# Kernel optimization log

Measured on AMD Instinct MI355X. Metric: run time of the kernel, lower is better.

## Reference

```python
import jax, jax.numpy as jnp
import numpy as np

EMBED_DIM = 768
NUM_HEADS = 12
HEAD_DIM = EMBED_DIM // NUM_HEADS
B, T = 2, 2048


def setup_inputs() -> dict:
    key = jax.random.key(0)
    kx, kq, kqb, ko, kob = jax.random.split(key, 5)
    x = jax.random.normal(kx, (B, T, EMBED_DIM), dtype=jnp.float32)
    # xavier-uniform style params
    lim_qkv = float(np.sqrt(6.0 / (EMBED_DIM + 3 * EMBED_DIM)))
    qkv_kernel = jax.random.uniform(kq, (EMBED_DIM, 3 * EMBED_DIM), minval=-lim_qkv, maxval=lim_qkv, dtype=jnp.float32)
    qkv_bias = jnp.zeros((3 * EMBED_DIM,), dtype=jnp.float32)
    lim_o = float(np.sqrt(6.0 / (EMBED_DIM + EMBED_DIM)))
    o_kernel = jax.random.uniform(ko, (EMBED_DIM, EMBED_DIM), minval=-lim_o, maxval=lim_o, dtype=jnp.float32)
    o_bias = jnp.zeros((EMBED_DIM,), dtype=jnp.float32)
    return {"x": x, "qkv_kernel": qkv_kernel, "qkv_bias": qkv_bias, "o_kernel": o_kernel, "o_bias": o_bias}


def reference(x, qkv_kernel, qkv_bias, o_kernel, o_bias):
    b, t, d = x.shape
    # fused QKV projection
    qkv = jnp.einsum('btd,de->bte', x, qkv_kernel) + qkv_bias  # [B,T,3D]
    qkv = qkv.reshape(b, t, 3, NUM_HEADS, HEAD_DIM).transpose(2, 0, 3, 1, 4)  # [3,B,H,T,Dh]
    q, k, v = qkv[0], qkv[1], qkv[2]
    # naive attention: materializes full [B,H,T,T] scores (as in original)
    scale = 1.0 / np.sqrt(HEAD_DIM).astype(np.float32)
    attn_logits = jnp.einsum('bhqd,bhkd->bhqk', q, k) * scale
    attention = jax.nn.softmax(attn_logits, axis=-1)
    values = jnp.einsum('bhqk,bhkd->bhqd', attention, v)
    values = values.transpose(0, 2, 1, 3).reshape(b, t, d)  # [B,T,D]
    o = jnp.einsum('btd,de->bte', values, o_kernel) + o_bias
    return (o, attention)
```

## Files before the change

kernel.cpp:

```cpp
#include <hip/hip_runtime.h>
#include <hip/hip_bf16.h>
#include <hip/hip_fp16.h>

typedef _Float16 f16;
typedef _Float16 f16x4 __attribute__((ext_vector_type(4)));
typedef _Float16 f16x8 __attribute__((ext_vector_type(8)));
typedef float f32x4 __attribute__((ext_vector_type(4)));

#define MFMA16(a, b, c) __builtin_amdgcn_mfma_f32_16x16x32_f16(a, b, c, 0, 0, 0)

__device__ __forceinline__ float fexp2(float x) {
#if __has_builtin(__builtin_amdgcn_exp2f)
    return __builtin_amdgcn_exp2f(x);
#else
    return exp2f(x);
#endif
}

__global__ void k_convert_x(const float* __restrict__ in, f16* __restrict__ out, int n4) {
    int i = blockIdx.x * blockDim.x + threadIdx.x;
    if (i >= n4) return;
    float4 v = ((const float4*)in)[i];
    f16x4 o = {(f16)v.x, (f16)v.y, (f16)v.z, (f16)v.w};
    ((f16x4*)out)[i] = o;
}

__global__ __launch_bounds__(256) void k_transpose(const float* __restrict__ in,
                                                   f16* __restrict__ out, int K, int N) {
    __shared__ f16 tile[64][72];
    int n0 = blockIdx.x * 64, k0 = blockIdx.y * 64;
    int t = threadIdx.x;
    int r = t >> 2, cb = (t & 3) * 16;
    const float* src = in + (size_t)(k0 + r) * N + n0 + cb;
#pragma unroll
    for (int j = 0; j < 4; ++j) {
        float4 v = ((const float4*)src)[j];
        tile[r][cb + 4 * j + 0] = (f16)v.x;
        tile[r][cb + 4 * j + 1] = (f16)v.y;
        tile[r][cb + 4 * j + 2] = (f16)v.z;
        tile[r][cb + 4 * j + 3] = (f16)v.w;
    }
    __syncthreads();
    int nl = t >> 2, kb = (t & 3) * 16;
    f16* dst = out + (size_t)(n0 + nl) * K + k0 + kb;
#pragma unroll
    for (int j = 0; j < 2; ++j) {
        f16x8 o;
#pragma unroll
        for (int e = 0; e < 8; ++e) o[e] = tile[kb + 8 * j + e][nl];
        *(f16x8*)(dst + 8 * j) = o;
    }
}

__device__ __forceinline__ void gemm_core(const f16* __restrict__ A, const f16* __restrict__ Bt,
                                          int m0, int n0, int t, int lane, int wr, int wc,
                                          f16* As, f16* Bs, f32x4 acc[4][4]) {
    for (int kt = 0; kt < 24; ++kt) {
#pragma unroll
        for (int i = 0; i < 2; ++i) {
            int c = t + i * 256;
            int row = c >> 2, cb = (c & 3) * 8;
            f16x8 va = *(const f16x8*)(A + (size_t)(m0 + row) * 768 + kt * 32 + cb);
            f16x8 vb = *(const f16x8*)(Bt + (size_t)(n0 + row) * 768 + kt * 32 + cb);
            *(f16x8*)(As + row * 40 + cb) = va;
            *(f16x8*)(Bs + row * 40 + cb) = vb;
        }
        __syncthreads();
        f16x8 a[4], b[4];
#pragma unroll
        for (int i = 0; i < 4; ++i)
            a[i] = *(const f16x8*)(As + (wr * 64 + i * 16 + (lane & 15)) * 40 + (lane >> 4) * 8);
#pragma unroll
        for (int j = 0; j < 4; ++j)
            b[j] = *(const f16x8*)(Bs + (wc * 64 + j * 16 + (lane & 15)) * 40 + (lane >> 4) * 8);
#pragma unroll
        for (int i = 0; i < 4; ++i)
#pragma unroll
            for (int j = 0; j < 4; ++j) acc[i][j] = MFMA16(a[i], b[j], acc[i][j]);
        __syncthreads();
    }
}

__global__ __launch_bounds__(256) void k_qkv_gemm(const f16* __restrict__ A, const f16* __restrict__ Bt,
                                                  const float* __restrict__ bias,
                                                  f16* __restrict__ Qh, f16* __restrict__ Kf,
                                                  f16* __restrict__ Vf) {
    __shared__ f16 As[128 * 40];
    __shared__ f16 Bs[128 * 40];
    int m0 = blockIdx.x * 128, n0 = blockIdx.y * 128;
    int t = threadIdx.x, lane = t & 63, w = t >> 6;
    int wr = w >> 1, wc = w & 1;
    f32x4 zero = {0.f, 0.f, 0.f, 0.f};
    f32x4 acc[4][4];
#pragma unroll
    for (int i = 0; i < 4; ++i)
#pragma unroll
        for (int j = 0; j < 4; ++j) acc[i][j] = zero;

    gemm_core(A, Bt, m0, n0, t, lane, wr, wc, As, Bs, acc);

    const float QSCALE = 0.18033688011112042f;
#pragma unroll
    for (int j = 0; j < 4; ++j) {
        int n = n0 + wc * 64 + j * 16 + (lane & 15);
        int which = n / 768;
        int rem = n - which * 768;
        int h = rem >> 6, d = rem & 63;
        float bv = bias[n];
#pragma unroll
        for (int i = 0; i < 4; ++i) {
            int m = m0 + wr * 64 + i * 16 + ((lane >> 4) << 2);
            int bb = m >> 11, tt = m & 2047;
            int bh = bb * 12 + h;
            if (which == 2) {
                int kt = tt >> 6;
                int half = (tt & 63) >> 5, hi = (tt & 31) >> 3, e0 = tt & 7;
                int jd = d >> 4, lo = d & 15;
                size_t addr = (((size_t)bh * 32 + kt) * 8 + jd * 2 + half) * 512 +
                              (size_t)(hi * 16 + lo) * 8 + e0;
                f16x4 pk;
#pragma unroll
                for (int r = 0; r < 4; ++r) pk[r] = (f16)(acc[i][j][r] + bv);
                *(f16x4*)(Vf + addr) = pk;
            } else if (which == 0) {
#pragma unroll
                for (int r = 0; r < 4; ++r)
                    Qh[((size_t)bh * 2048 + tt + r) * 64 + d] = (f16)((acc[i][j][r] + bv) * QSCALE);
            } else {
                int half = d >> 5, hi = (d & 31) >> 3, e = d & 7;
#pragma unroll
                for (int r = 0; r < 4; ++r) {
                    int tr = tt + r;
                    int kt = tr >> 6, row = tr & 63;
                    int s = row >> 4, lo = row & 15;
                    size_t addr = (((size_t)bh * 32 + kt) * 8 + s * 2 + half) * 512 +
                                  (size_t)(hi * 16 + lo) * 8 + e;
                    Kf[addr] = (f16)(acc[i][j][r] + bv);
                }
            }
        }
    }
}

__global__ __launch_bounds__(256) void k_o_gemm(const f16* __restrict__ A, const f16* __restrict__ Bt,
                                                const float* __restrict__ bias,
                                                float* __restrict__ out) {
    __shared__ f16 As[128 * 40];
    __shared__ f16 Bs[128 * 40];
    int m0 = blockIdx.x * 128, n0 = blockIdx.y * 128;
    int t = threadIdx.x, lane = t & 63, w = t >> 6;
    int wr = w >> 1, wc = w & 1;
    f32x4 zero = {0.f, 0.f, 0.f, 0.f};
    f32x4 acc[4][4];
#pragma unroll
    for (int i = 0; i < 4; ++i)
#pragma unroll
        for (int j = 0; j < 4; ++j) acc[i][j] = zero;

    gemm_core(A, Bt, m0, n0, t, lane, wr, wc, As, Bs, acc);

#pragma unroll
    for (int j = 0; j < 4; ++j) {
        int n = n0 + wc * 64 + j * 16 + (lane & 15);
        float bv = bias[n];
#pragma unroll
        for (int i = 0; i < 4; ++i) {
            int m = m0 + wr * 64 + i * 16 + ((lane >> 4) << 2);
#pragma unroll
            for (int r = 0; r < 4; ++r) out[(size_t)(m + r) * 768 + n] = acc[i][j][r] + bv;
        }
    }
}

__global__ __launch_bounds__(256, 3) void k_attn(const f16* __restrict__ Qh, const f16* __restrict__ Kf,
                                                 const f16* __restrict__ Vf, float* __restrict__ attn,
                                                 f16* __restrict__ valh) {
    __shared__ __align__(16) float Ps32_all[4][16 * 68];
    int orig = blockIdx.x;
    int swz = (orig & 7) * 96 + (orig >> 3);
    int bh = swz >> 5, qt = swz & 31;
    int q0 = qt * 64;
    int t = threadIdx.x, lane = t & 63, w = t >> 6;

    const f16* qbase = Qh + ((size_t)bh * 2048 + q0 + w * 16) * 64;
    const f16* kfb = Kf + (size_t)bh * 32 * 4096 + (size_t)lane * 8;
    const f16* vfb = Vf + (size_t)bh * 32 * 4096 + (size_t)lane * 8;

    f16x8 aq[2];
#pragma unroll
    for (int f = 0; f < 2; ++f)
        aq[f] = *(const f16x8*)(qbase + (size_t)(lane & 15) * 64 + f * 32 + (lane >> 4) * 8);

    f32x4 zero = {0.f, 0.f, 0.f, 0.f};

    auto LOADK = [&](f16x8* dst, int kt) {
        const f16* kp = kfb + (size_t)kt * 4096;
#pragma unroll
        for (int f = 0; f < 8; ++f) dst[f] = *(const f16x8*)(kp + f * 512);
    };
    auto LOADV = [&](f16x8* dst, int kt) {
        const f16* vp = vfb + (size_t)kt * 4096;
#pragma unroll
        for (int f = 0; f < 8; ++f) dst[f] = *(const f16x8*)(vp + f * 512);
    };
    auto QKT = [&](const f16x8* kf, f32x4* s4) {
#pragma unroll
        for (int s = 0; s < 4; ++s) {
            s4[s] = MFMA16(aq[0], kf[2 * s], zero);
            s4[s] = MFMA16(aq[1], kf[2 * s + 1], s4[s]);
        }
    };

    f16x8 ka[8], kb2[8];

    float lsum[4] = {0.f, 0.f, 0.f, 0.f};
    LOADK(ka, 0);
    for (int kt = 0; kt < 32; kt += 2) {
        f32x4 s4[4];
        LOADK(kb2, kt + 1);
        QKT(ka, s4);
#pragma unroll
        for (int s = 0; s < 4; ++s)
#pragma unroll
            for (int r = 0; r < 4; ++r) lsum[r] += fexp2(s4[s][r]);
        LOADK(ka, (kt + 2) & 31);
        QKT(kb2, s4);
#pragma unroll
        for (int s = 0; s < 4; ++s)
#pragma unroll
            for (int r = 0; r < 4; ++r) lsum[r] += fexp2(s4[s][r]);
    }
#pragma unroll
    for (int r = 0; r < 4; ++r) {
#pragma unroll
        for (int off = 1; off < 16; off <<= 1) lsum[r] += __shfl_xor(lsum[r], off, 64);
    }
    float linv[4];
#pragma unroll
    for (int r = 0; r < 4; ++r) linv[r] = 1.0f / lsum[r];

    f32x4 accv[4];
#pragma unroll
    for (int j = 0; j < 4; ++j) accv[j] = zero;
    float* Ps = Ps32_all[w];
    float* attn_base = attn + ((size_t)bh * 2048 + q0 + w * 16) * 2048;
    f16x8 vbuf[8];

    auto step2 = [&](f16x8* curK, f16x8* nxtK, int kt) {
        LOADV(vbuf, kt);
        LOADK(nxtK, (kt + 1) & 31);
        f32x4 s4[4];
        QKT(curK, s4);
#pragma unroll
        for (int s = 0; s < 4; ++s) {
#pragma unroll
            for (int r = 0; r < 4; ++r) {
                float p = fexp2(s4[s][r]) * linv[r];
                Ps[((lane >> 4) * 4 + r) * 68 + s * 16 + (lane & 15)] = p;
            }
        }
        f16x8 pa[2];
#pragma unroll
        for (int half = 0; half < 2; ++half) {
            const float* pr = Ps + (lane & 15) * 68 + half * 32 + (lane >> 4) * 8;
            f32x4 lo = *(const f32x4*)(pr);
            f32x4 hi = *(const f32x4*)(pr + 4);
            f16x8 pf = {(f16)lo[0], (f16)lo[1], (f16)lo[2], (f16)lo[3],
                        (f16)hi[0], (f16)hi[1], (f16)hi[2], (f16)hi[3]};
            pa[half] = pf;
        }
        float* ab = attn_base + kt * 64;
#pragma unroll
        for (int i = 0; i < 4; ++i) {
            int row = i * 4 + (lane >> 4);
            int col = (lane & 15) * 4;
            f32x4 v = *(const f32x4*)(Ps + row * 68 + col);
            *(f32x4*)(ab + (size_t)row * 2048 + col) = v;
        }
#pragma unroll
        for (int jd = 0; jd < 4; ++jd) {
            accv[jd] = MFMA16(pa[0], vbuf[2 * jd], accv[jd]);
            accv[jd] = MFMA16(pa[1], vbuf[2 * jd + 1], accv[jd]);
        }
    };

    LOADK(ka, 0);
    for (int kt = 0; kt < 32; kt += 2) {
        step2(ka, kb2, kt);
        step2(kb2, ka, kt + 1);
    }

    int b = bh / 12, h = bh - b * 12;
#pragma unroll
    for (int j = 0; j < 4; ++j) {
#pragma unroll
        for (int r = 0; r < 4; ++r) {
            int rowg = b * 2048 + q0 + w * 16 + (lane >> 4) * 4 + r;
            int col = h * 64 + j * 16 + (lane & 15);
            valh[(size_t)rowg * 768 + col] = (f16)accv[j][r];
        }
    }
}

extern "C" void kernel_launch(void* const* d_in, const int* in_sizes, int n_in,
                              void* d_out, int out_size, void* d_ws, size_t ws_size,
                              hipStream_t stream) {
    const float* x = (const float*)d_in[0];
    const float* wqkv = (const float*)d_in[1];
    const float* bqkv = (const float*)d_in[2];
    const float* wo = (const float*)d_in[3];
    const float* bo = (const float*)d_in[4];

    float* out_o = (float*)d_out;
    float* out_attn = out_o + (size_t)2 * 2048 * 768;

    f16* ws = (f16*)d_ws;
    f16* xh = ws;
    f16* wqkv_t = xh + 3145728;
    f16* wo_t = wqkv_t + 1769472;
    f16* Qh = wo_t + 589824;
    f16* Kf = Qh + 3145728;
    f16* Vf = Kf + 3145728;
    f16* valh = Vf + 3145728;

    k_convert_x<<<3072, 256, 0, stream>>>(x, xh, 786432);
    k_transpose<<<dim3(36, 12), 256, 0, stream>>>(wqkv, wqkv_t, 768, 2304);
    k_transpose<<<dim3(12, 12), 256, 0, stream>>>(wo, wo_t, 768, 768);
    k_qkv_gemm<<<dim3(32, 18), 256, 0, stream>>>(xh, wqkv_t, bqkv, Qh, Kf, Vf);
    k_attn<<<768, 256, 0, stream>>>(Qh, Kf, Vf, out_attn, valh);
    k_o_gemm<<<dim3(32, 6), 256, 0, stream>>>(valh, wo_t, bo, out_o);
}
```

Measured before the change: 200.7 us.

## Split softmax row-sum pass into separate parallel kernel and use direct-to-LDS GEMM loads

```diff
diff --git a/kernel.cpp b/kernel.cpp
--- a/kernel.cpp
+++ b/kernel.cpp
@@ -15,6 +15,12 @@
 #else
     return exp2f(x);
 #endif
+}
+
+typedef __attribute__((address_space(1))) const void gconst_t;
+typedef __attribute__((address_space(3))) void lds_t;
+__device__ __forceinline__ void gload16(const f16* g, f16* l) {
+    __builtin_amdgcn_global_load_lds((gconst_t*)g, (lds_t*)l, 16, 0, 0);
 }
 
 __global__ void k_convert_x(const float* __restrict__ in, f16* __restrict__ out, int n4) {
@@ -53,26 +59,25 @@
 }
 
 __device__ __forceinline__ void gemm_core(const f16* __restrict__ A, const f16* __restrict__ Bt,
-                                          int m0, int n0, int t, int lane, int wr, int wc,
+                                          int m0, int n0, int lane, int w, int wr, int wc,
                                           f16* As, f16* Bs, f32x4 acc[4][4]) {
+    int srow = lane >> 2;
+    int scol = (lane & 3) * 8;
     for (int kt = 0; kt < 24; ++kt) {
-#pragma unroll
-        for (int i = 0; i < 2; ++i) {
-            int c = t + i * 256;
-            int row = c >> 2, cb = (c & 3) * 8;
-            f16x8 va = *(const f16x8*)(A + (size_t)(m0 + row) * 768 + kt * 32 + cb);
-            f16x8 vb = *(const f16x8*)(Bt + (size_t)(n0 + row) * 768 + kt * 32 + cb);
-            *(f16x8*)(As + row * 40 + cb) = va;
-            *(f16x8*)(Bs + row * 40 + cb) = vb;
-        }
+        const f16* ab = A + (size_t)(m0 + w * 32 + srow) * 768 + kt * 32 + scol;
+        const f16* bb = Bt + (size_t)(n0 + w * 32 + srow) * 768 + kt * 32 + scol;
+        gload16(ab, As + (w * 32) * 32);
+        gload16(ab + (size_t)16 * 768, As + (w * 32 + 16) * 32);
+        gload16(bb, Bs + (w * 32) * 32);
+        gload16(bb + (size_t)16 * 768, Bs + (w * 32 + 16) * 32);
         __syncthreads();
         f16x8 a[4], b[4];
 #pragma unroll
         for (int i = 0; i < 4; ++i)
-            a[i] = *(const f16x8*)(As + (wr * 64 + i * 16 + (lane & 15)) * 40 + (lane >> 4) * 8);
+            a[i] = *(const f16x8*)(As + (wr * 64 + i * 16 + (lane & 15)) * 32 + (lane >> 4) * 8);
 #pragma unroll
         for (int j = 0; j < 4; ++j)
-            b[j] = *(const f16x8*)(Bs + (wc * 64 + j * 16 + (lane & 15)) * 40 + (lane >> 4) * 8);
+            b[j] = *(const f16x8*)(Bs + (wc * 64 + j * 16 + (lane & 15)) * 32 + (lane >> 4) * 8);
 #pragma unroll
         for (int i = 0; i < 4; ++i)
 #pragma unroll
@@ -85,8 +90,8 @@
                                                   const float* __restrict__ bias,
                                                   f16* __restrict__ Qh, f16* __restrict__ Kf,
                                                   f16* __restrict__ Vf) {
-    __shared__ f16 As[128 * 40];
-    __shared__ f16 Bs[128 * 40];
+    __shared__ __align__(16) f16 As[128 * 32];
+    __shared__ __align__(16) f16 Bs[128 * 32];
     int m0 = blockIdx.x * 128, n0 = blockIdx.y * 128;
     int t = threadIdx.x, lane = t & 63, w = t >> 6;
     int wr = w >> 1, wc = w & 1;
@@ -97,7 +102,7 @@
 #pragma unroll
         for (int j = 0; j < 4; ++j) acc[i][j] = zero;
 
-    gemm_core(A, Bt, m0, n0, t, lane, wr, wc, As, Bs, acc);
+    gemm_core(A, Bt, m0, n0, lane, w, wr, wc, As, Bs, acc);
 
     const float QSCALE = 0.18033688011112042f;
 #pragma unroll
@@ -145,8 +150,8 @@
 __global__ __launch_bounds__(256) void k_o_gemm(const f16* __restrict__ A, const f16* __restrict__ Bt,
                                                 const float* __restrict__ bias,
                                                 float* __restrict__ out) {
-    __shared__ f16 As[128 * 40];
-    __shared__ f16 Bs[128 * 40];
+    __shared__ __align__(16) f16 As[128 * 32];
+    __shared__ __align__(16) f16 Bs[128 * 32];
     int m0 = blockIdx.x * 128, n0 = blockIdx.y * 128;
     int t = threadIdx.x, lane = t & 63, w = t >> 6;
     int wr = w >> 1, wc = w & 1;
@@ -157,7 +162,7 @@
 #pragma unroll
         for (int j = 0; j < 4; ++j) acc[i][j] = zero;
 
-    gemm_core(A, Bt, m0, n0, t, lane, wr, wc, As, Bs, acc);
+    gemm_core(A, Bt, m0, n0, lane, w, wr, wc, As, Bs, acc);
 
 #pragma unroll
     for (int j = 0; j < 4; ++j) {
@@ -172,9 +177,68 @@
     }
 }
 
+__global__ __launch_bounds__(256) void k_lsum(const f16* __restrict__ Qh, const f16* __restrict__ Kf,
+                                              float* __restrict__ lpart) {
+    int qt = blockIdx.x, bh = blockIdx.y, kc = blockIdx.z;
+    int q0 = qt * 64;
+    int t = threadIdx.x, lane = t & 63, w = t >> 6;
+    const f16* qbase = Qh + ((size_t)bh * 2048 + q0 + w * 16) * 64;
+    const f16* kfb = Kf + (size_t)bh * 32 * 4096 + (size_t)lane * 8;
+
+    f16x8 aq[2];
+#pragma unroll
+    for (int f = 0; f < 2; ++f)
+        aq[f] = *(const f16x8*)(qbase + (size_t)(lane & 15) * 64 + f * 32 + (lane >> 4) * 8);
+    f32x4 zero = {0.f, 0.f, 0.f, 0.f};
+
+    auto LOADK = [&](f16x8* dst, int kt) {
+        const f16* kp = kfb + (size_t)kt * 4096;
+#pragma unroll
+        for (int f = 0; f < 8; ++f) dst[f] = *(const f16x8*)(kp + f * 512);
+    };
+    auto QKT = [&](const f16x8* kf, f32x4* s4) {
+#pragma unroll
+        for (int s = 0; s < 4; ++s) {
+            s4[s] = MFMA16(aq[0], kf[2 * s], zero);
+            s4[s] = MFMA16(aq[1], kf[2 * s + 1], s4[s]);
+        }
+    };
+
+    f16x8 ka[8], kb2[8];
+    float lsum[4] = {0.f, 0.f, 0.f, 0.f};
+    int base = kc * 8;
+    LOADK(ka, base);
+    for (int i = 0; i < 8; i += 2) {
+        f32x4 s4[4];
+        LOADK(kb2, base + i + 1);
+        QKT(ka, s4);
+#pragma unroll
+        for (int s = 0; s < 4; ++s)
+#pragma unroll
+            for (int r = 0; r < 4; ++r) lsum[r] += fexp2(s4[s][r]);
+        LOADK(ka, base + ((i + 2) & 7));
+        QKT(kb2, s4);
+#pragma unroll
+        for (int s = 0; s < 4; ++s)
+#pragma unroll
+            for (int r = 0; r < 4; ++r) lsum[r] += fexp2(s4[s][r]);
+    }
+#pragma unroll
+    for (int r = 0; r < 4; ++r) {
+#pragma unroll
+        for (int off = 1; off < 16; off <<= 1) lsum[r] += __shfl_xor(lsum[r], off, 64);
+    }
+    int qrow = q0 + w * 16 + (lane >> 4) * 4;
+    float* lp = lpart + (size_t)kc * 49152 + (size_t)bh * 2048;
+#pragma unroll
+    for (int r = 0; r < 4; ++r)
+        if ((lane & 15) == r) lp[qrow + r] = lsum[r];
+}
+
 __global__ __launch_bounds__(256, 3) void k_attn(const f16* __restrict__ Qh, const f16* __restrict__ Kf,
-                                                 const f16* __restrict__ Vf, float* __restrict__ attn,
-                                                 f16* __restrict__ valh) {
+                                                 const f16* __restrict__ Vf,
+                                                 const float* __restrict__ lpart,
+                                                 float* __restrict__ attn, f16* __restrict__ valh) {
     __shared__ __align__(16) float Ps32_all[4][16 * 68];
     int orig = blockIdx.x;
     int swz = (orig & 7) * 96 + (orig >> 3);
@@ -190,18 +254,23 @@
 #pragma unroll
     for (int f = 0; f < 2; ++f)
         aq[f] = *(const f16x8*)(qbase + (size_t)(lane & 15) * 64 + f * 32 + (lane >> 4) * 8);
-
     f32x4 zero = {0.f, 0.f, 0.f, 0.f};
+
+    int qrow = q0 + w * 16 + (lane >> 4) * 4;
+    float linv[4];
+#pragma unroll
+    for (int r = 0; r < 4; ++r) {
+        float s = 0.f;
+#pragma unroll
+        for (int kc = 0; kc < 4; ++kc)
+            s += lpart[(size_t)kc * 49152 + (size_t)bh * 2048 + qrow + r];
+        linv[r] = 1.0f / s;
+    }
 
     auto LOADK = [&](f16x8* dst, int kt) {
         const f16* kp = kfb + (size_t)kt * 4096;
 #pragma unroll
         for (int f = 0; f < 8; ++f) dst[f] = *(const f16x8*)(kp + f * 512);
-    };
-    auto LOADV = [&](f16x8* dst, int kt) {
-        const f16* vp = vfb + (size_t)kt * 4096;
-#pragma unroll
-        for (int f = 0; f < 8; ++f) dst[f] = *(const f16x8*)(vp + f * 512);
     };
     auto QKT = [&](const f16x8* kf, f32x4* s4) {
 #pragma unroll
@@ -211,43 +280,19 @@
         }
     };
 
-    f16x8 ka[8], kb2[8];
-
-    float lsum[4] = {0.f, 0.f, 0.f, 0.f};
-    LOADK(ka, 0);
-    for (int kt = 0; kt < 32; kt += 2) {
-        f32x4 s4[4];
-        LOADK(kb2, kt + 1);
-        QKT(ka, s4);
-#pragma unroll
-        for (int s = 0; s < 4; ++s)
-#pragma unroll
-            for (int r = 0; r < 4; ++r) lsum[r] += fexp2(s4[s][r]);
-        LOADK(ka, (kt + 2) & 31);
-        QKT(kb2, s4);
-#pragma unroll
-        for (int s = 0; s < 4; ++s)
-#pragma unroll
-            for (int r = 0; r < 4; ++r) lsum[r] += fexp2(s4[s][r]);
-    }
-#pragma unroll
-    for (int r = 0; r < 4; ++r) {
-#pragma unroll
-        for (int off = 1; off < 16; off <<= 1) lsum[r] += __shfl_xor(lsum[r], off, 64);
-    }
-    float linv[4];
-#pragma unroll
-    for (int r = 0; r < 4; ++r) linv[r] = 1.0f / lsum[r];
-
     f32x4 accv[4];
 #pragma unroll
     for (int j = 0; j < 4; ++j) accv[j] = zero;
     float* Ps = Ps32_all[w];
     float* attn_base = attn + ((size_t)bh * 2048 + q0 + w * 16) * 2048;
-    f16x8 vbuf[8];
+    f16x8 ka[8], kb2[8], vbuf[8];
 
     auto step2 = [&](f16x8* curK, f16x8* nxtK, int kt) {
-        LOADV(vbuf, kt);
+        {
+            const f16* vp = vfb + (size_t)kt * 4096;
+#pragma unroll
+            for (int f = 0; f < 8; ++f) vbuf[f] = *(const f16x8*)(vp + f * 512);
+        }
         LOADK(nxtK, (kt + 1) & 31);
         f32x4 s4[4];
         QKT(curK, s4);
@@ -322,11 +367,13 @@
     f16* Kf = Qh + 3145728;
     f16* Vf = Kf + 3145728;
     f16* valh = Vf + 3145728;
+    float* lpart = (float*)(valh + 3145728);
 
     k_convert_x<<<3072, 256, 0, stream>>>(x, xh, 786432);
     k_transpose<<<dim3(36, 12), 256, 0, stream>>>(wqkv, wqkv_t, 768, 2304);
     k_transpose<<<dim3(12, 12), 256, 0, stream>>>(wo, wo_t, 768, 768);
     k_qkv_gemm<<<dim3(32, 18), 256, 0, stream>>>(xh, wqkv_t, bqkv, Qh, Kf, Vf);
-    k_attn<<<768, 256, 0, stream>>>(Qh, Kf, Vf, out_attn, valh);
+    k_lsum<<<dim3(32, 24, 4), 256, 0, stream>>>(Qh, Kf, lpart);
+    k_attn<<<768, 256, 0, stream>>>(Qh, Kf, Vf, lpart, out_attn, valh);
     k_o_gemm<<<dim3(32, 6), 256, 0, stream>>>(valh, wo_t, bo, out_o);
 }
```

Measured after the change: 216.7 us. 7.9% more time.

## Split attention into row-sum pass and key-split pass with partial outputs

Applied to the files above, without the earlier changes.

```diff
diff --git a/kernel.cpp b/kernel.cpp
--- a/kernel.cpp
+++ b/kernel.cpp
@@ -142,7 +142,8 @@
     }
 }
 
-__global__ __launch_bounds__(256) void k_o_gemm(const f16* __restrict__ A, const f16* __restrict__ Bt,
+__global__ __launch_bounds__(256) void k_o_gemm(const float* __restrict__ P0, const float* __restrict__ P1,
+                                                const f16* __restrict__ Bt,
                                                 const float* __restrict__ bias,
                                                 float* __restrict__ out) {
     __shared__ f16 As[128 * 40];
@@ -157,7 +158,35 @@
 #pragma unroll
         for (int j = 0; j < 4; ++j) acc[i][j] = zero;
 
-    gemm_core(A, Bt, m0, n0, t, lane, wr, wc, As, Bs, acc);
+    for (int kt = 0; kt < 24; ++kt) {
+#pragma unroll
+        for (int i = 0; i < 2; ++i) {
+            int c = t + i * 256;
+            int row = c >> 2, cb = (c & 3) * 8;
+            const float* a0 = P0 + (size_t)(m0 + row) * 768 + kt * 32 + cb;
+            const float* a1 = P1 + (size_t)(m0 + row) * 768 + kt * 32 + cb;
+            f32x4 u0 = *(const f32x4*)a0 + *(const f32x4*)a1;
+            f32x4 u1 = *(const f32x4*)(a0 + 4) + *(const f32x4*)(a1 + 4);
+            f16x8 av = {(f16)u0[0], (f16)u0[1], (f16)u0[2], (f16)u0[3],
+                        (f16)u1[0], (f16)u1[1], (f16)u1[2], (f16)u1[3]};
+            *(f16x8*)(As + row * 40 + cb) = av;
+            f16x8 vb = *(const f16x8*)(Bt + (size_t)(n0 + row) * 768 + kt * 32 + cb);
+            *(f16x8*)(Bs + row * 40 + cb) = vb;
+        }
+        __syncthreads();
+        f16x8 a[4], b[4];
+#pragma unroll
+        for (int i = 0; i < 4; ++i)
+            a[i] = *(const f16x8*)(As + (wr * 64 + i * 16 + (lane & 15)) * 40 + (lane >> 4) * 8);
+#pragma unroll
+        for (int j = 0; j < 4; ++j)
+            b[j] = *(const f16x8*)(Bs + (wc * 64 + j * 16 + (lane & 15)) * 40 + (lane >> 4) * 8);
+#pragma unroll
+        for (int i = 0; i < 4; ++i)
+#pragma unroll
+            for (int j = 0; j < 4; ++j) acc[i][j] = MFMA16(a[i], b[j], acc[i][j]);
+        __syncthreads();
+    }
 
 #pragma unroll
     for (int j = 0; j < 4; ++j) {
@@ -172,13 +201,74 @@
     }
 }
 
-__global__ __launch_bounds__(256, 3) void k_attn(const f16* __restrict__ Qh, const f16* __restrict__ Kf,
-                                                 const f16* __restrict__ Vf, float* __restrict__ attn,
-                                                 f16* __restrict__ valh) {
-    __shared__ __align__(16) float Ps32_all[4][16 * 68];
+__global__ __launch_bounds__(256) void k_lsum(const f16* __restrict__ Qh, const f16* __restrict__ Kf,
+                                              float* __restrict__ lpart) {
     int orig = blockIdx.x;
-    int swz = (orig & 7) * 96 + (orig >> 3);
-    int bh = swz >> 5, qt = swz & 31;
+    int swz = (orig & 7) * 384 + (orig >> 3);
+    int bh = swz >> 7, rem = swz & 127, qt = rem >> 2, kc = rem & 3;
+    int q0 = qt * 64;
+    int t = threadIdx.x, lane = t & 63, w = t >> 6;
+    const f16* qbase = Qh + ((size_t)bh * 2048 + q0 + w * 16) * 64;
+    const f16* kfb = Kf + (size_t)bh * 32 * 4096 + (size_t)lane * 8;
+
+    f16x8 aq[2];
+#pragma unroll
+    for (int f = 0; f < 2; ++f)
+        aq[f] = *(const f16x8*)(qbase + (size_t)(lane & 15) * 64 + f * 32 + (lane >> 4) * 8);
+    f32x4 zero = {0.f, 0.f, 0.f, 0.f};
+
+    auto LOADK = [&](f16x8* dst, int kt) {
+        const f16* kp = kfb + (size_t)kt * 4096;
+#pragma unroll
+        for (int f = 0; f < 8; ++f) dst[f] = *(const f16x8*)(kp + f * 512);
+    };
+    auto QKT = [&](const f16x8* kf, f32x4* s4) {
+#pragma unroll
+        for (int s = 0; s < 4; ++s) {
+            s4[s] = MFMA16(aq[0], kf[2 * s], zero);
+            s4[s] = MFMA16(aq[1], kf[2 * s + 1], s4[s]);
+        }
+    };
+
+    f16x8 ka[8], kb2[8];
+    float lsum[4] = {0.f, 0.f, 0.f, 0.f};
+    int base = kc * 8;
+    LOADK(ka, base);
+    for (int i = 0; i < 8; i += 2) {
+        f32x4 s4[4];
+        LOADK(kb2, base + i + 1);
+        QKT(ka, s4);
+#pragma unroll
+        for (int s = 0; s < 4; ++s)
+#pragma unroll
+            for (int r = 0; r < 4; ++r) lsum[r] += fexp2(s4[s][r]);
+        LOADK(ka, base + ((i + 2) & 7));
+        QKT(kb2, s4);
+#pragma unroll
+        for (int s = 0; s < 4; ++s)
+#pragma unroll
+            for (int r = 0; r < 4; ++r) lsum[r] += fexp2(s4[s][r]);
+    }
+#pragma unroll
+    for (int r = 0; r < 4; ++r) {
+#pragma unroll
+        for (int off = 1; off < 16; off <<= 1) lsum[r] += __shfl_xor(lsum[r], off, 64);
+    }
+    int qrow = q0 + w * 16 + (lane >> 4) * 4;
+    float* lp = lpart + (size_t)kc * 49152 + (size_t)bh * 2048;
+#pragma unroll
+    for (int r = 0; r < 4; ++r)
+        if ((lane & 15) == r) lp[qrow + r] = lsum[r];
+}
+
+__global__ __launch_bounds__(256, 4) void k_attn(const f16* __restrict__ Qh, const f16* __restrict__ Kf,
+                                                 const f16* __restrict__ Vf,
+                                                 const float* __restrict__ lpart,
+                                                 float* __restrict__ attn, float* __restrict__ valp) {
+    __shared__ __align__(16) float Ps32_all[4][16 * 36];
+    int orig = blockIdx.x;
+    int swz = (orig & 7) * 192 + (orig >> 3);
+    int bh = swz >> 6, rem = swz & 63, qt = rem >> 1, kc2 = rem & 1;
     int q0 = qt * 64;
     int t = threadIdx.x, lane = t & 63, w = t >> 6;
 
@@ -190,114 +280,90 @@
 #pragma unroll
     for (int f = 0; f < 2; ++f)
         aq[f] = *(const f16x8*)(qbase + (size_t)(lane & 15) * 64 + f * 32 + (lane >> 4) * 8);
-
     f32x4 zero = {0.f, 0.f, 0.f, 0.f};
 
-    auto LOADK = [&](f16x8* dst, int kt) {
-        const f16* kp = kfb + (size_t)kt * 4096;
-#pragma unroll
-        for (int f = 0; f < 8; ++f) dst[f] = *(const f16x8*)(kp + f * 512);
+    int qrow = q0 + w * 16 + (lane >> 4) * 4;
+    float linv[4];
+#pragma unroll
+    for (int r = 0; r < 4; ++r) {
+        float s = 0.f;
+#pragma unroll
+        for (int kc = 0; kc < 4; ++kc)
+            s += lpart[(size_t)kc * 49152 + (size_t)bh * 2048 + qrow + r];
+        linv[r] = 1.0f / s;
+    }
+
+    auto LOADK32 = [&](f16x8* dst, int ks) {
+        const f16* p = kfb + (size_t)ks * 2048;
+#pragma unroll
+        for (int f = 0; f < 4; ++f) dst[f] = *(const f16x8*)(p + f * 512);
     };
-    auto LOADV = [&](f16x8* dst, int kt) {
-        const f16* vp = vfb + (size_t)kt * 4096;
-#pragma unroll
-        for (int f = 0; f < 8; ++f) dst[f] = *(const f16x8*)(vp + f * 512);
+    auto LOADV32 = [&](f16x8* dst, int ks) {
+        const f16* p = vfb + (size_t)(ks >> 1) * 4096 + (size_t)(ks & 1) * 512;
+#pragma unroll
+        for (int jd = 0; jd < 4; ++jd) dst[jd] = *(const f16x8*)(p + jd * 1024);
     };
-    auto QKT = [&](const f16x8* kf, f32x4* s4) {
-#pragma unroll
-        for (int s = 0; s < 4; ++s) {
-            s4[s] = MFMA16(aq[0], kf[2 * s], zero);
-            s4[s] = MFMA16(aq[1], kf[2 * s + 1], s4[s]);
-        }
-    };
-
-    f16x8 ka[8], kb2[8];
-
-    float lsum[4] = {0.f, 0.f, 0.f, 0.f};
-    LOADK(ka, 0);
-    for (int kt = 0; kt < 32; kt += 2) {
-        f32x4 s4[4];
-        LOADK(kb2, kt + 1);
-        QKT(ka, s4);
-#pragma unroll
-        for (int s = 0; s < 4; ++s)
-#pragma unroll
-            for (int r = 0; r < 4; ++r) lsum[r] += fexp2(s4[s][r]);
-        LOADK(ka, (kt + 2) & 31);
-        QKT(kb2, s4);
-#pragma unroll
-        for (int s = 0; s < 4; ++s)
-#pragma unroll
-            for (int r = 0; r < 4; ++r) lsum[r] += fexp2(s4[s][r]);
-    }
-#pragma unroll
-    for (int r = 0; r < 4; ++r) {
-#pragma unroll
-        for (int off = 1; off < 16; off <<= 1) lsum[r] += __shfl_xor(lsum[r], off, 64);
-    }
-    float linv[4];
-#pragma unroll
-    for (int r = 0; r < 4; ++r) linv[r] = 1.0f / lsum[r];
 
     f32x4 accv[4];
 #pragma unroll
     for (int j = 0; j < 4; ++j) accv[j] = zero;
     float* Ps = Ps32_all[w];
     float* attn_base = attn + ((size_t)bh * 2048 + q0 + w * 16) * 2048;
-    f16x8 vbuf[8];
-
-    auto step2 = [&](f16x8* curK, f16x8* nxtK, int kt) {
-        LOADV(vbuf, kt);
-        LOADK(nxtK, (kt + 1) & 31);
-        f32x4 s4[4];
-        QKT(curK, s4);
-#pragma unroll
-        for (int s = 0; s < 4; ++s) {
+    f16x8 ka[4], kb2[4], vbuf[4];
+    int base = kc2 * 32;
+
+    auto step2 = [&](f16x8* curK, f16x8* nxtK, int ks) {
+        LOADV32(vbuf, ks);
+        LOADK32(nxtK, base + (((ks + 1) - base) & 31));
+        f32x4 s4[2];
+        s4[0] = MFMA16(aq[0], curK[0], zero);
+        s4[0] = MFMA16(aq[1], curK[1], s4[0]);
+        s4[1] = MFMA16(aq[0], curK[2], zero);
+        s4[1] = MFMA16(aq[1], curK[3], s4[1]);
+#pragma unroll
+        for (int sp = 0; sp < 2; ++sp) {
 #pragma unroll
             for (int r = 0; r < 4; ++r) {
-                float p = fexp2(s4[s][r]) * linv[r];
-                Ps[((lane >> 4) * 4 + r) * 68 + s * 16 + (lane & 15)] = p;
+                float p = fexp2(s4[sp][r]) * linv[r];
+                Ps[((lane >> 4) * 4 + r) * 36 + sp * 16 + (lane & 15)] = p;
             }
         }
-        f16x8 pa[2];
-#pragma unroll
-        for (int half = 0; half < 2; ++half) {
-            const float* pr = Ps + (lane & 15) * 68 + half * 32 + (lane >> 4) * 8;
+        f16x8 pa;
+        {
+            const float* pr = Ps + (lane & 15) * 36 + (lane >> 4) * 8;
             f32x4 lo = *(const f32x4*)(pr);
             f32x4 hi = *(const f32x4*)(pr + 4);
             f16x8 pf = {(f16)lo[0], (f16)lo[1], (f16)lo[2], (f16)lo[3],
                         (f16)hi[0], (f16)hi[1], (f16)hi[2], (f16)hi[3]};
-            pa[half] = pf;
-        }
-        float* ab = attn_base + kt * 64;
-#pragma unroll
-        for (int i = 0; i < 4; ++i) {
-            int row = i * 4 + (lane >> 4);
-            int col = (lane & 15) * 4;
-            f32x4 v = *(const f32x4*)(Ps + row * 68 + col);
+            pa = pf;
+        }
+        float* ab = attn_base + ks * 32;
+#pragma unroll
+        for (int i = 0; i < 2; ++i) {
+            int row = i * 8 + (lane >> 3);
+            int col = (lane & 7) * 4;
+            f32x4 v = *(const f32x4*)(Ps + row * 36 + col);
             *(f32x4*)(ab + (size_t)row * 2048 + col) = v;
         }
 #pragma unroll
-        for (int jd = 0; jd < 4; ++jd) {
-            accv[jd] = MFMA16(pa[0], vbuf[2 * jd], accv[jd]);
-            accv[jd] = MFMA16(pa[1], vbuf[2 * jd + 1], accv[jd]);
-        }
+        for (int jd = 0; jd < 4; ++jd) accv[jd] = MFMA16(pa, vbuf[jd], accv[jd]);
     };
 
-    LOADK(ka, 0);
-    for (int kt = 0; kt < 32; kt += 2) {
-        step2(ka, kb2, kt);
-        step2(kb2, ka, kt + 1);
+    LOADK32(ka, base);
+    for (int i = 0; i < 32; i += 2) {
+        step2(ka, kb2, base + i);
+        step2(kb2, ka, base + i + 1);
     }
 
     int b = bh / 12, h = bh - b * 12;
+    float* vp = valp + (size_t)kc2 * 3145728;
 #pragma unroll
     for (int j = 0; j < 4; ++j) {
 #pragma unroll
         for (int r = 0; r < 4; ++r) {
             int rowg = b * 2048 + q0 + w * 16 + (lane >> 4) * 4 + r;
             int col = h * 64 + j * 16 + (lane & 15);
-            valh[(size_t)rowg * 768 + col] = (f16)accv[j][r];
+            vp[(size_t)rowg * 768 + col] = accv[j][r];
         }
     }
 }
@@ -321,12 +387,14 @@
     f16* Qh = wo_t + 589824;
     f16* Kf = Qh + 3145728;
     f16* Vf = Kf + 3145728;
-    f16* valh = Vf + 3145728;
+    float* lpart = (float*)(Vf + 3145728);
+    float* valp = lpart + 196608;
 
     k_convert_x<<<3072, 256, 0, stream>>>(x, xh, 786432);
     k_transpose<<<dim3(36, 12), 256, 0, stream>>>(wqkv, wqkv_t, 768, 2304);
     k_transpose<<<dim3(12, 12), 256, 0, stream>>>(wo, wo_t, 768, 768);
     k_qkv_gemm<<<dim3(32, 18), 256, 0, stream>>>(xh, wqkv_t, bqkv, Qh, Kf, Vf);
-    k_attn<<<768, 256, 0, stream>>>(Qh, Kf, Vf, out_attn, valh);
-    k_o_gemm<<<dim3(32, 6), 256, 0, stream>>>(valh, wo_t, bo, out_o);
-}
+    k_lsum<<<3072, 256, 0, stream>>>(Qh, Kf, lpart);
+    k_attn<<<1536, 256, 0, stream>>>(Qh, Kf, Vf, lpart, out_attn, valp);
+    k_o_gemm<<<dim3(32, 6), 256, 0, stream>>>(valp, valp + 3145728, wo_t, bo, out_o);
+}
```

Measured after the change: 255.4 us. 1.27x slower.
